# Kernel optimization log

Hardware: AMD Instinct MI355X
Metric: run time of the kernel (lower is better)

The kernel has to match this reference:

```python
import jax, jax.numpy as jnp
import numpy as np

HEADS = 8
DIM_HEAD = 40
QUERY_DIM = 320          # == inner_dim = HEADS * DIM_HEAD
CONTEXT_DIM = 768
INNER = HEADS * DIM_HEAD


def setup_inputs() -> dict:
    key = jax.random.key(0)
    ks = jax.random.split(key, 8)
    B, NQ, NK = 32, 4096, 77
    s_q = 1.0 / np.sqrt(QUERY_DIM)
    s_c = 1.0 / np.sqrt(CONTEXT_DIM)
    s_i = 1.0 / np.sqrt(INNER)
    return {
        "x": jax.random.normal(ks[0], (B, NQ, QUERY_DIM), jnp.float32),
        "context": jax.random.normal(ks[1], (B, NK, CONTEXT_DIM), jnp.float32),
        "Wq": jax.random.normal(ks[2], (INNER, QUERY_DIM), jnp.float32) * s_q,
        "Wk": jax.random.normal(ks[3], (INNER, CONTEXT_DIM), jnp.float32) * s_c,
        "Wv": jax.random.normal(ks[4], (INNER, CONTEXT_DIM), jnp.float32) * s_c,
        "Wo": jax.random.normal(ks[5], (QUERY_DIM, INNER), jnp.float32) * s_i,
        "bo": jnp.zeros((QUERY_DIM,), jnp.float32),
        "gamma_q": jnp.ones((INNER,), jnp.float32),
        "gamma_k": jnp.ones((INNER,), jnp.float32),
        "gamma_v": jnp.ones((INNER,), jnp.float32),
        "gamma_out": jnp.ones((INNER,), jnp.float32),
    }


def reference(x, context, Wq, Wk, Wv, Wo, bo, gamma_q, gamma_k, gamma_v, gamma_out):
    B, NQ, _ = x.shape
    NK = context.shape[1]
    # linear projections (bias=False) followed by per-channel gamma scaling
    q = (x @ Wq.T) * gamma_q            # [B, NQ, INNER]
    k = (context @ Wk.T) * gamma_k      # [B, NK, INNER]
    v = (context @ Wv.T) * gamma_v      # [B, NK, INNER]
    # split heads: b n (h d) -> b h n d
    q = q.reshape(B, NQ, HEADS, DIM_HEAD).transpose(0, 2, 1, 3)
    k = k.reshape(B, NK, HEADS, DIM_HEAD).transpose(0, 2, 1, 3)
    v = v.reshape(B, NK, HEADS, DIM_HEAD).transpose(0, 2, 1, 3)
    scale = DIM_HEAD ** -0.5
    scores = jnp.einsum("bhqd,bhkd->bhqk", q, k) * scale  # [B,H,NQ,NK]
    attn = jax.nn.softmax(scores, axis=-1)
    o = jnp.einsum("bhqk,bhkd->bhqd", attn, v)            # [B,H,NQ,Dh]
    o = o.transpose(0, 2, 1, 3).reshape(B, NQ, INNER)
    # output projection (with bias) then gamma_out scale; dropout p=0 -> identity
    return (o @ Wo.T + bo) * gamma_out
```

## Files before the change

kernel.cpp:

```cpp
#include <hip/hip_runtime.h>

#define B_   32
#define NQ_  4096
#define NK_  77
#define H_   8
#define DH_  40
#define IN_  320
#define CD_  768
#define M_   (B_ * NQ_)
#define MKV_ (B_ * NK_)

#define NKP_  80
#define NKP2_ 96
#define DHP_  48
#define KQ_   64

typedef __attribute__((ext_vector_type(8))) short bf16x8;
typedef __attribute__((ext_vector_type(4))) float f32x4;
typedef unsigned short ushort_t;

__device__ __forceinline__ unsigned short f2bf(float f) {
  union { float f; unsigned int i; } v; v.f = f;
  unsigned int i = v.i;
  i += 0x7fffu + ((i >> 16) & 1u);
  return (unsigned short)(i >> 16);
}
__device__ __forceinline__ unsigned int pack2(float a, float b) {
  return (unsigned int)f2bf(a) | ((unsigned int)f2bf(b) << 16);
}

__global__ __launch_bounds__(256) void wcvt(
    const float* __restrict__ Wq, const float* __restrict__ Wo,
    const float* __restrict__ Wk, const float* __restrict__ Wv,
    unsigned short* __restrict__ Wqb, unsigned short* __restrict__ Wob,
    unsigned short* __restrict__ Wkb, unsigned short* __restrict__ Wvb)
{
  const int i = blockIdx.x * 256 + threadIdx.x;
  const float* src;
  unsigned short* dst;
  int n;
  switch (blockIdx.y) {
    case 0:  src = Wq; dst = Wqb; n = IN_ * IN_ / 4; break;
    case 1:  src = Wo; dst = Wob; n = IN_ * IN_ / 4; break;
    case 2:  src = Wk; dst = Wkb; n = IN_ * CD_ / 4; break;
    default: src = Wv; dst = Wvb; n = IN_ * CD_ / 4; break;
  }
  if (i >= n) return;
  const float4 v = ((const float4*)src)[i];
  uint2 p; p.x = pack2(v.x, v.y); p.y = pack2(v.z, v.w);
  ((uint2*)dst)[i] = p;
}

__global__ __launch_bounds__(256) void kv_mfma(
    const float* __restrict__ ctx, const unsigned short* __restrict__ Wkb,
    const unsigned short* __restrict__ Wvb, const float* __restrict__ gk,
    const float* __restrict__ gv, unsigned short* __restrict__ Khb,
    unsigned short* __restrict__ Vtb)
{
  constexpr int LDA = 40;
  __shared__ alignas(16) unsigned short As[64 * LDA];
  __shared__ alignas(16) unsigned short Bs[64 * LDA];
  const int m0 = blockIdx.x * 64;
  const int n0 = blockIdx.y * 64;
  const int isV = blockIdx.z;
  const unsigned short* Wb = isV ? Wvb : Wkb;
  const int tid = threadIdx.x;
  const int wave = tid >> 6;
  const int lane = tid & 63;
  const int lm = lane & 15;
  const int quad = lane >> 4;

  f32x4 acc0 = {0.f, 0.f, 0.f, 0.f};
  f32x4 acc1 = acc0, acc2 = acc0, acc3 = acc0;

  for (int k0 = 0; k0 < CD_; k0 += 32) {
#pragma unroll
    for (int c = tid; c < 512; c += 256) {
      const int row = c >> 3, kq = (c & 7) << 2;
      const int fr = m0 + row;
      float4 v = {0.f, 0.f, 0.f, 0.f};
      if (fr < MKV_)
        v = *(const float4*)(ctx + (size_t)fr * CD_ + k0 + kq);
      uint2 p; p.x = pack2(v.x, v.y); p.y = pack2(v.z, v.w);
      *(uint2*)(&As[row * LDA + kq]) = p;
    }
    {
      const int row = tid >> 2, kq = (tid & 3) << 3;
      *(uint4*)(&Bs[row * LDA + kq]) =
          *(const uint4*)(Wb + (size_t)(n0 + row) * CD_ + k0 + kq);
    }
    __syncthreads();
    const bf16x8 a  = *(const bf16x8*)(&As[(wave * 16 + lm) * LDA + quad * 8]);
    const bf16x8 b0 = *(const bf16x8*)(&Bs[( 0 + lm) * LDA + quad * 8]);
    const bf16x8 b1 = *(const bf16x8*)(&Bs[(16 + lm) * LDA + quad * 8]);
    const bf16x8 b2 = *(const bf16x8*)(&Bs[(32 + lm) * LDA + quad * 8]);
    const bf16x8 b3 = *(const bf16x8*)(&Bs[(48 + lm) * LDA + quad * 8]);
    acc0 = __builtin_amdgcn_mfma_f32_16x16x32_bf16(a, b0, acc0, 0, 0, 0);
    acc1 = __builtin_amdgcn_mfma_f32_16x16x32_bf16(a, b1, acc1, 0, 0, 0);
    acc2 = __builtin_amdgcn_mfma_f32_16x16x32_bf16(a, b2, acc2, 0, 0, 0);
    acc3 = __builtin_amdgcn_mfma_f32_16x16x32_bf16(a, b3, acc3, 0, 0, 0);
    __syncthreads();
  }

  const float* g = isV ? gv : gk;
  const f32x4 accs[4] = {acc0, acc1, acc2, acc3};
#pragma unroll
  for (int t = 0; t < 4; ++t) {
    const int col = n0 + t * 16 + lm;
    const int h = col / DH_, d = col % DH_;
    const float gc = g[col];
#pragma unroll
    for (int r = 0; r < 4; ++r) {
      const int row = m0 + wave * 16 + quad * 4 + r;
      if (row < MKV_) {
        const int bb = row / NK_, pos = row % NK_;
        const unsigned short val = f2bf(accs[t][r] * gc);
        if (!isV)
          Khb[((size_t)(bb * H_ + h) * NKP_ + pos) * KQ_ + d] = val;
        else
          Vtb[((size_t)(bb * H_ + h) * DHP_ + d) * NKP2_ + pos] = val;
      }
    }
  }
}

template <int MODE>
__global__ __launch_bounds__(256) void gemm_proj(
    const void* __restrict__ Ap, const unsigned short* __restrict__ Wb,
    const float* __restrict__ gamma, const float* __restrict__ bias,
    void* __restrict__ Cp)
{
  constexpr int LDA = 40;
  __shared__ alignas(16) unsigned short As[64 * LDA];
  __shared__ alignas(16) unsigned short Bs[64 * LDA];
  const int m0 = blockIdx.x * 64;
  const int n0 = blockIdx.y * 64;
  const int tid = threadIdx.x;
  const int wave = tid >> 6;
  const int lane = tid & 63;
  const int lm = lane & 15;
  const int quad = lane >> 4;

  f32x4 acc0 = {0.f, 0.f, 0.f, 0.f};
  f32x4 acc1 = acc0, acc2 = acc0, acc3 = acc0;

  for (int k0 = 0; k0 < IN_; k0 += 32) {
    if (MODE == 0) {
      const float* A = (const float*)Ap;
#pragma unroll
      for (int c = tid; c < 512; c += 256) {
        const int row = c >> 3, kq = (c & 7) << 2;
        const float4 v = *(const float4*)(A + (size_t)(m0 + row) * IN_ + k0 + kq);
        uint2 p; p.x = pack2(v.x, v.y); p.y = pack2(v.z, v.w);
        *(uint2*)(&As[row * LDA + kq]) = p;
      }
    } else {
      const unsigned short* A = (const unsigned short*)Ap;
      const int row = tid >> 2, kq = (tid & 3) << 3;
      *(uint4*)(&As[row * LDA + kq]) =
          *(const uint4*)(A + (size_t)(m0 + row) * IN_ + k0 + kq);
    }
    {
      const int row = tid >> 2, kq = (tid & 3) << 3;
      *(uint4*)(&Bs[row * LDA + kq]) =
          *(const uint4*)(Wb + (size_t)(n0 + row) * IN_ + k0 + kq);
    }
    __syncthreads();
    const bf16x8 a  = *(const bf16x8*)(&As[(wave * 16 + lm) * LDA + quad * 8]);
    const bf16x8 b0 = *(const bf16x8*)(&Bs[( 0 + lm) * LDA + quad * 8]);
    const bf16x8 b1 = *(const bf16x8*)(&Bs[(16 + lm) * LDA + quad * 8]);
    const bf16x8 b2 = *(const bf16x8*)(&Bs[(32 + lm) * LDA + quad * 8]);
    const bf16x8 b3 = *(const bf16x8*)(&Bs[(48 + lm) * LDA + quad * 8]);
    acc0 = __builtin_amdgcn_mfma_f32_16x16x32_bf16(a, b0, acc0, 0, 0, 0);
    acc1 = __builtin_amdgcn_mfma_f32_16x16x32_bf16(a, b1, acc1, 0, 0, 0);
    acc2 = __builtin_amdgcn_mfma_f32_16x16x32_bf16(a, b2, acc2, 0, 0, 0);
    acc3 = __builtin_amdgcn_mfma_f32_16x16x32_bf16(a, b3, acc3, 0, 0, 0);
    __syncthreads();
  }

  const f32x4 accs[4] = {acc0, acc1, acc2, acc3};
#pragma unroll
  for (int t = 0; t < 4; ++t) {
#pragma unroll
    for (int r = 0; r < 4; ++r) {
      const int row = m0 + wave * 16 + quad * 4 + r;
      const int col = n0 + t * 16 + lm;
      const float v = accs[t][r];
      if (MODE == 0) {
        ((unsigned short*)Cp)[(size_t)row * IN_ + col] = f2bf(v * gamma[col]);
      } else {
        ((float*)Cp)[(size_t)row * IN_ + col] = (v + bias[col]) * gamma[col];
      }
    }
  }
}

#define QT_ 128
__global__ __launch_bounds__(256) void attn_mfma(
    const unsigned short* __restrict__ Khb,
    const unsigned short* __restrict__ Vtb,
    unsigned short* __restrict__ QO)
{
  __shared__ alignas(16) unsigned short smem[14976 + 48 * 104];
  unsigned short* Qs = smem;
  unsigned short* Ks = smem + 128 * 72;
  unsigned short* Vt = smem + 14976;
  unsigned short* Ps = smem;

  const int b = blockIdx.z, h = blockIdx.y, qt = blockIdx.x;
  const int tid = threadIdx.x;
  const int row0 = qt * QT_;
  const size_t qbase = ((size_t)b * NQ_ + row0) * IN_ + h * DH_;

  for (int i = tid; i < QT_ * 9; i += 256) {
    const int row = i / 9, seg = i % 9;
    uint4 v = {0u, 0u, 0u, 0u};
    if (seg < 5)
      v = *(const uint4*)(QO + qbase + (size_t)row * IN_ + seg * 8);
    *(uint4*)(&Qs[row * 72 + seg * 8]) = v;
  }
  {
    const unsigned short* src = Khb + (size_t)(b * H_ + h) * NKP_ * KQ_;
    for (int i = tid; i < NKP_ * 9; i += 256) {
      const int row = i / 9, seg = i % 9;
      uint4 v = {0u, 0u, 0u, 0u};
      if (seg < 8) v = *(const uint4*)(src + row * KQ_ + seg * 8);
      *(uint4*)(&Ks[row * 72 + seg * 8]) = v;
    }
  }
  {
    const unsigned short* src = Vtb + (size_t)(b * H_ + h) * DHP_ * NKP2_;
    for (int i = tid; i < DHP_ * 12; i += 256) {
      const int row = i / 12, seg = i % 12;
      *(uint4*)(&Vt[row * 104 + seg * 8]) =
          *(const uint4*)(src + row * NKP2_ + seg * 8);
    }
  }
  __syncthreads();

  const int wave = tid >> 6;
  const int lane = tid & 63;
  const int lm = lane & 15;
  const int quad = lane >> 4;
  const int wrow = wave * 32;

  f32x4 sacc[2][5];
#pragma unroll
  for (int mf = 0; mf < 2; ++mf)
#pragma unroll
    for (int t = 0; t < 5; ++t) sacc[mf][t] = (f32x4){0.f, 0.f, 0.f, 0.f};

#pragma unroll
  for (int k = 0; k < 2; ++k) {
    bf16x8 aq[2];
#pragma unroll
    for (int mf = 0; mf < 2; ++mf)
      aq[mf] = *(const bf16x8*)(&Qs[(wrow + mf * 16 + lm) * 72 + k * 32 + quad * 8]);
#pragma unroll
    for (int t = 0; t < 5; ++t) {
      const bf16x8 bk = *(const bf16x8*)(&Ks[(t * 16 + lm) * 72 + k * 32 + quad * 8]);
#pragma unroll
      for (int mf = 0; mf < 2; ++mf)
        sacc[mf][t] = __builtin_amdgcn_mfma_f32_16x16x32_bf16(aq[mf], bk, sacc[mf][t], 0, 0, 0);
    }
  }

  const float scale = 0.15811388300841897f;
  float sv[2][5][4];
  float rl[2][4];
#pragma unroll
  for (int mf = 0; mf < 2; ++mf) {
#pragma unroll
    for (int t = 0; t < 5; ++t)
#pragma unroll
      for (int r = 0; r < 4; ++r) {
        float v = sacc[mf][t][r] * scale;
        if (t == 4 && lm >= 13) v = -1e30f;
        sv[mf][t][r] = v;
      }
#pragma unroll
    for (int r = 0; r < 4; ++r) {
      float m = sv[mf][0][r];
#pragma unroll
      for (int t = 1; t < 5; ++t) m = fmaxf(m, sv[mf][t][r]);
#pragma unroll
      for (int d = 1; d < 16; d <<= 1) m = fmaxf(m, __shfl_xor(m, d));
      float l = 0.f;
#pragma unroll
      for (int t = 0; t < 5; ++t) {
        const float e = __expf(sv[mf][t][r] - m);
        sv[mf][t][r] = e;
        l += e;
      }
#pragma unroll
      for (int d = 1; d < 16; d <<= 1) l += __shfl_xor(l, d);
      rl[mf][r] = 1.f / l;
    }
  }

  __syncthreads();

  unsigned short* Pw = Ps + wave * 32 * 104;
#pragma unroll
  for (int mf = 0; mf < 2; ++mf)
#pragma unroll
    for (int t = 0; t < 5; ++t)
#pragma unroll
      for (int r = 0; r < 4; ++r)
        Pw[(mf * 16 + quad * 4 + r) * 104 + t * 16 + lm] = f2bf(sv[mf][t][r]);
  {
    const int row = lane >> 1, half = lane & 1;
    *(uint4*)(&Pw[row * 104 + 80 + half * 8]) = (uint4){0u, 0u, 0u, 0u};
  }
  __syncthreads();

  f32x4 oacc[2][3];
#pragma unroll
  for (int mf = 0; mf < 2; ++mf)
#pragma unroll
    for (int n = 0; n < 3; ++n) oacc[mf][n] = (f32x4){0.f, 0.f, 0.f, 0.f};

#pragma unroll
  for (int k = 0; k < 3; ++k) {
    bf16x8 ap[2];
#pragma unroll
    for (int mf = 0; mf < 2; ++mf)
      ap[mf] = *(const bf16x8*)(&Pw[(mf * 16 + lm) * 104 + k * 32 + quad * 8]);
#pragma unroll
    for (int n = 0; n < 3; ++n) {
      const bf16x8 bv = *(const bf16x8*)(&Vt[(n * 16 + lm) * 104 + k * 32 + quad * 8]);
#pragma unroll
      for (int mf = 0; mf < 2; ++mf)
        oacc[mf][n] = __builtin_amdgcn_mfma_f32_16x16x32_bf16(ap[mf], bv, oacc[mf][n], 0, 0, 0);
    }
  }

#pragma unroll
  for (int mf = 0; mf < 2; ++mf)
#pragma unroll
    for (int n = 0; n < 3; ++n) {
      const int col = n * 16 + lm;
      if (col < DH_) {
#pragma unroll
        for (int r = 0; r < 4; ++r) {
          const int row = wrow + mf * 16 + quad * 4 + r;
          QO[qbase + (size_t)row * IN_ + col] = f2bf(oacc[mf][n][r] * rl[mf][r]);
        }
      }
    }
}

extern "C" void kernel_launch(void* const* d_in, const int* in_sizes, int n_in,
                              void* d_out, int out_size, void* d_ws,
                              size_t ws_size, hipStream_t stream)
{
  const float* x   = (const float*)d_in[0];
  const float* ctx = (const float*)d_in[1];
  const float* Wq  = (const float*)d_in[2];
  const float* Wk  = (const float*)d_in[3];
  const float* Wv  = (const float*)d_in[4];
  const float* Wo  = (const float*)d_in[5];
  const float* bo  = (const float*)d_in[6];
  const float* gq  = (const float*)d_in[7];
  const float* gk  = (const float*)d_in[8];
  const float* gv  = (const float*)d_in[9];
  const float* go  = (const float*)d_in[10];
  float* out = (float*)d_out;

  char* ws = (char*)d_ws;
  unsigned short* q_ws = (unsigned short*)ws;
  size_t off = (size_t)M_ * IN_ * 2;
  unsigned short* Khb = (unsigned short*)(ws + off); off += (size_t)B_ * H_ * NKP_ * KQ_ * 2;
  unsigned short* Vtb = (unsigned short*)(ws + off); off += (size_t)B_ * H_ * DHP_ * NKP2_ * 2;
  unsigned short* Wqb = (unsigned short*)(ws + off); off += (size_t)IN_ * IN_ * 2;
  unsigned short* Wob = (unsigned short*)(ws + off);
  unsigned short* Wkb = (unsigned short*)ws;
  unsigned short* Wvb = (unsigned short*)(ws + (size_t)IN_ * CD_ * 2);

  hipMemsetAsync(Khb, 0, (size_t)B_ * H_ * NKP_ * KQ_ * 2, stream);
  hipMemsetAsync(Vtb, 0, (size_t)B_ * H_ * DHP_ * NKP2_ * 2, stream);

  wcvt<<<dim3(IN_ * CD_ / 4 / 256, 4), dim3(256), 0, stream>>>(
      Wq, Wo, Wk, Wv, Wqb, Wob, Wkb, Wvb);
  kv_mfma<<<dim3((MKV_ + 63) / 64, IN_ / 64, 2), dim3(256), 0, stream>>>(
      ctx, Wkb, Wvb, gk, gv, Khb, Vtb);
  gemm_proj<0><<<dim3(M_ / 64, IN_ / 64), dim3(256), 0, stream>>>(
      x, Wqb, gq, nullptr, q_ws);
  attn_mfma<<<dim3(NQ_ / QT_, H_, B_), dim3(256), 0, stream>>>(Khb, Vtb, q_ws);
  gemm_proj<1><<<dim3(M_ / 64, IN_ / 64), dim3(256), 0, stream>>>(
      q_ws, Wob, go, bo, out);
}
```

Before: 596.8 us.

## Restructure projection GEMMs into full-row strips with register-resident A

Each block now owns a 64-row strip of the output across all 320 columns. The A fragments for the whole K=320 are loaded once into registers, converted from fp32 when needed, and the weight matrix is staged in shared memory in five 64-column chunks. Before, A was re-read for each of the five N-tiles and every 32-wide K step needed two barriers. The change trades that for higher register pressure (ten bf16x8 fragments per thread), a larger shared buffer, and five times fewer blocks in the grid.

Measured after the change: 486.7 us. -18.4%, faster.

```diff
diff --git a/kernel.cpp b/kernel.cpp
--- a/kernel.cpp
+++ b/kernel.cpp
@@ -125,71 +125,87 @@
 }
 
 template <int MODE>
-__global__ __launch_bounds__(256) void gemm_proj(
+__global__ __launch_bounds__(256) void gemm_strip(
     const void* __restrict__ Ap, const unsigned short* __restrict__ Wb,
     const float* __restrict__ gamma, const float* __restrict__ bias,
     void* __restrict__ Cp)
 {
-  constexpr int LDA = 40;
-  __shared__ alignas(16) unsigned short As[64 * LDA];
-  __shared__ alignas(16) unsigned short Bs[64 * LDA];
+  constexpr int LDB = 328;
+  __shared__ alignas(16) unsigned short Bs[64 * LDB];
   const int m0 = blockIdx.x * 64;
-  const int n0 = blockIdx.y * 64;
   const int tid = threadIdx.x;
   const int wave = tid >> 6;
   const int lane = tid & 63;
   const int lm = lane & 15;
   const int quad = lane >> 4;
-
-  f32x4 acc0 = {0.f, 0.f, 0.f, 0.f};
-  f32x4 acc1 = acc0, acc2 = acc0, acc3 = acc0;
-
-  for (int k0 = 0; k0 < IN_; k0 += 32) {
-    if (MODE == 0) {
-      const float* A = (const float*)Ap;
-#pragma unroll
-      for (int c = tid; c < 512; c += 256) {
-        const int row = c >> 3, kq = (c & 7) << 2;
-        const float4 v = *(const float4*)(A + (size_t)(m0 + row) * IN_ + k0 + kq);
-        uint2 p; p.x = pack2(v.x, v.y); p.y = pack2(v.z, v.w);
-        *(uint2*)(&As[row * LDA + kq]) = p;
-      }
-    } else {
-      const unsigned short* A = (const unsigned short*)Ap;
-      const int row = tid >> 2, kq = (tid & 3) << 3;
-      *(uint4*)(&As[row * LDA + kq]) =
-          *(const uint4*)(A + (size_t)(m0 + row) * IN_ + k0 + kq);
-    }
+  const int arow = m0 + wave * 16 + lm;
+
+  bf16x8 a[10];
+  if (MODE == 0) {
+    const float* A = (const float*)Ap;
+#pragma unroll
+    for (int kf = 0; kf < 10; ++kf) {
+      const float* p = A + (size_t)arow * IN_ + kf * 32 + quad * 8;
+      const float4 v0 = *(const float4*)(p);
+      const float4 v1 = *(const float4*)(p + 4);
+      union { uint4 u; bf16x8 h; } cv;
+      cv.u.x = pack2(v0.x, v0.y); cv.u.y = pack2(v0.z, v0.w);
+      cv.u.z = pack2(v1.x, v1.y); cv.u.w = pack2(v1.z, v1.w);
+      a[kf] = cv.h;
+    }
+  } else {
+    const unsigned short* A = (const unsigned short*)Ap;
+#pragma unroll
+    for (int kf = 0; kf < 10; ++kf)
+      a[kf] = *(const bf16x8*)(A + (size_t)arow * IN_ + kf * 32 + quad * 8);
+  }
+
+  const int srow = tid >> 2;
+  const int sc0 = tid & 3;
+
+  for (int nc = 0; nc < 5; ++nc) {
+    if (nc) __syncthreads();
     {
-      const int row = tid >> 2, kq = (tid & 3) << 3;
-      *(uint4*)(&Bs[row * LDA + kq]) =
-          *(const uint4*)(Wb + (size_t)(n0 + row) * IN_ + k0 + kq);
+      const unsigned short* src = Wb + (size_t)(nc * 64 + srow) * IN_;
+      unsigned short* dst = &Bs[srow * LDB];
+#pragma unroll
+      for (int j = 0; j < 10; ++j) {
+        const int c = (sc0 + j * 4) * 8;
+        *(uint4*)(dst + c) = *(const uint4*)(src + c);
+      }
     }
     __syncthreads();
-    const bf16x8 a  = *(const bf16x8*)(&As[(wave * 16 + lm) * LDA + quad * 8]);
-    const bf16x8 b0 = *(const bf16x8*)(&Bs[( 0 + lm) * LDA + quad * 8]);
-    const bf16x8 b1 = *(const bf16x8*)(&Bs[(16 + lm) * LDA + quad * 8]);
-    const bf16x8 b2 = *(const bf16x8*)(&Bs[(32 + lm) * LDA + quad * 8]);
-    const bf16x8 b3 = *(const bf16x8*)(&Bs[(48 + lm) * LDA + quad * 8]);
-    acc0 = __builtin_amdgcn_mfma_f32_16x16x32_bf16(a, b0, acc0, 0, 0, 0);
-    acc1 = __builtin_amdgcn_mfma_f32_16x16x32_bf16(a, b1, acc1, 0, 0, 0);
-    acc2 = __builtin_amdgcn_mfma_f32_16x16x32_bf16(a, b2, acc2, 0, 0, 0);
-    acc3 = __builtin_amdgcn_mfma_f32_16x16x32_bf16(a, b3, acc3, 0, 0, 0);
-    __syncthreads();
-  }
-
-  const f32x4 accs[4] = {acc0, acc1, acc2, acc3};
-#pragma unroll
-  for (int t = 0; t < 4; ++t) {
-#pragma unroll
-    for (int r = 0; r < 4; ++r) {
-      const int row = m0 + wave * 16 + quad * 4 + r;
-      const int col = n0 + t * 16 + lm;
-      const float v = accs[t][r];
+
+    f32x4 acc[4];
+#pragma unroll
+    for (int nf = 0; nf < 4; ++nf) acc[nf] = (f32x4){0.f, 0.f, 0.f, 0.f};
+#pragma unroll
+    for (int kf = 0; kf < 10; ++kf) {
+#pragma unroll
+      for (int nf = 0; nf < 4; ++nf) {
+        const bf16x8 b =
+            *(const bf16x8*)(&Bs[(nf * 16 + lm) * LDB + kf * 32 + quad * 8]);
+        acc[nf] = __builtin_amdgcn_mfma_f32_16x16x32_bf16(a[kf], b, acc[nf], 0, 0, 0);
+      }
+    }
+
+#pragma unroll
+    for (int nf = 0; nf < 4; ++nf) {
+      const int col = nc * 64 + nf * 16 + lm;
+      const float g = gamma[col];
       if (MODE == 0) {
-        ((unsigned short*)Cp)[(size_t)row * IN_ + col] = f2bf(v * gamma[col]);
+#pragma unroll
+        for (int r = 0; r < 4; ++r) {
+          const int row = m0 + wave * 16 + quad * 4 + r;
+          ((unsigned short*)Cp)[(size_t)row * IN_ + col] = f2bf(acc[nf][r] * g);
+        }
       } else {
-        ((float*)Cp)[(size_t)row * IN_ + col] = (v + bias[col]) * gamma[col];
+        const float bb = bias[col];
+#pragma unroll
+        for (int r = 0; r < 4; ++r) {
+          const int row = m0 + wave * 16 + quad * 4 + r;
+          ((float*)Cp)[(size_t)row * IN_ + col] = (acc[nf][r] + bb) * g;
+        }
       }
     }
   }
@@ -384,9 +400,9 @@
       Wq, Wo, Wk, Wv, Wqb, Wob, Wkb, Wvb);
   kv_mfma<<<dim3((MKV_ + 63) / 64, IN_ / 64, 2), dim3(256), 0, stream>>>(
       ctx, Wkb, Wvb, gk, gv, Khb, Vtb);
-  gemm_proj<0><<<dim3(M_ / 64, IN_ / 64), dim3(256), 0, stream>>>(
+  gemm_strip<0><<<dim3(M_ / 64), dim3(256), 0, stream>>>(
       x, Wqb, gq, nullptr, q_ws);
   attn_mfma<<<dim3(NQ_ / QT_, H_, B_), dim3(256), 0, stream>>>(Khb, Vtb, q_ws);
-  gemm_proj<1><<<dim3(M_ / 64, IN_ / 64), dim3(256), 0, stream>>>(
+  gemm_strip<1><<<dim3(M_ / 64), dim3(256), 0, stream>>>(
       q_ws, Wob, go, bo, out);
 }
```
